# Kernel tuning notes

Hardware: AMD Instinct MI355X
Metric: run time of the kernel (lower is better)

## Reference

```python
import jax, jax.numpy as jnp
import numpy as np

DEPTH = 5  # init kwarg


def setup_inputs() -> dict:
    key = jax.random.key(0)
    ks = jax.random.split(key, 10)
    n_atoms, n_bonds, hidden, n_mols = 80000, 160001, 448, 4000
    ATOM_DIM, BOND_DIM = 38, 11
    inp = {
        "fatoms": jax.random.normal(ks[0], (n_atoms, ATOM_DIM), jnp.float32),
        "fbonds": jax.random.normal(ks[1], (n_bonds, ATOM_DIM + BOND_DIM), jnp.float32),
        "W_i": jax.random.normal(ks[2], (ATOM_DIM + BOND_DIM, hidden), jnp.float32) * 0.1,
        "W_h": jax.random.normal(ks[3], (hidden, hidden), jnp.float32) * 0.05,
        "W_o": jax.random.normal(ks[4], (ATOM_DIM + hidden, hidden), jnp.float32) * 0.05,
        "b_o": jax.random.normal(ks[5], (hidden,), jnp.float32),
        "agraph": jax.random.randint(ks[6], (n_atoms, 6), 0, n_bonds, jnp.int64),
        "bgraph": jax.random.randint(ks[7], (n_bonds, 6), 0, n_bonds, jnp.int64),
        "mol_idx": jnp.sort(jax.random.randint(ks[8], (n_atoms,), 0, n_mols, jnp.int64)),
        "n_mols": n_mols,
    }
    return inp


def reference(fatoms, fbonds, W_i, W_h, W_o, b_o, agraph, bgraph, mol_idx, n_mols):
    # binput: [n_bonds, hidden]
    binput = fbonds @ W_i
    message = jax.nn.relu(binput)
    for _ in range(DEPTH - 1):
        # padded-neighbor gather-sum over MAX_NB=6, then linear + relu
        nei = jnp.take(message, bgraph, axis=0).sum(axis=1)  # [n_bonds, hidden]
        message = jax.nn.relu(binput + nei @ W_h)
    # atom readout
    nei = jnp.take(message, agraph, axis=0).sum(axis=1)  # [n_atoms, hidden]
    ainput = jnp.concatenate([fatoms, nei], axis=1)
    atom_hiddens = jax.nn.relu(ainput @ W_o + b_o)
    # per-molecule mean pooling (scope -> segment ids)
    sums = jax.ops.segment_sum(atom_hiddens, mol_idx, num_segments=n_mols)
    counts = jax.ops.segment_sum(jnp.ones((atom_hiddens.shape[0],), atom_hiddens.dtype), mol_idx, num_segments=n_mols)
    return sums / jnp.maximum(counts, 1.0)[:, None]
```

## Files before the change

kernel.cpp:

```cpp
#include <hip/hip_runtime.h>

#define HIDDEN 448

typedef __attribute__((ext_vector_type(8))) short short8;
typedef __attribute__((ext_vector_type(4))) float f32x4;

__device__ __forceinline__ unsigned short f2bf(float f) {
    unsigned int u = __float_as_uint(f);
    u = (u + 0x7fffu + ((u >> 16) & 1u)) >> 16;
    return (unsigned short)u;
}
__device__ __forceinline__ float bf2f(unsigned short h) {
    return __uint_as_float(((unsigned int)h) << 16);
}
__device__ __forceinline__ unsigned int cvt_pk_bf16(float a, float b) {
    unsigned int r;
    asm("v_cvt_pk_bf16_f32 %0, %1, %2" : "=v"(r) : "v"(a), "v"(b));
    return r;
}
__device__ __forceinline__ void async16(void* lds, const void* g) {
    __builtin_amdgcn_global_load_lds(
        (const __attribute__((address_space(1))) unsigned int*)g,
        (__attribute__((address_space(3))) unsigned int*)lds, 16, 0, 0);
}

__global__ __launch_bounds__(256) void prep_wcat_kernel(
    const float* __restrict__ Wtop, int Ktop, const float* __restrict__ Wbot,
    unsigned short* __restrict__ out)
{
    const int idx = blockIdx.x * 256 + threadIdx.x;
    if (idx >= 448 * 512) return;
    const int n = idx >> 9, k = idx & 511;
    float v = 0.0f;
    if (k < Ktop) v = Wtop[k * HIDDEN + n];
    else if (k >= 64) v = Wbot[(k - 64) * HIDDEN + n];
    out[(size_t)n * 512 + (k ^ (((n >> 1) & 3) << 3))] = f2bf(v);
}

__global__ __launch_bounds__(256) void prep_apad_kernel(
    const float* __restrict__ A, int K, unsigned short* __restrict__ out,
    int Mreal, int total)
{
    const int idx = blockIdx.x * 256 + threadIdx.x;
    if (idx >= total) return;
    const int row = idx >> 6, k = idx & 63;
    const float v = (row < Mreal && k < K) ? A[(size_t)row * K + k] : 0.0f;
    out[(size_t)row * 64 + (k ^ (((row >> 1) & 3) << 3))] = f2bf(v);
}

template<int GRAPH, int OUTQ>
__global__ __launch_bounds__(512, 4) void gemm_mfma_kernel(
    const unsigned short* __restrict__ Apad,
    const unsigned char* __restrict__ Xq,
    const float* __restrict__ Xs,
    const int* __restrict__ graph,
    const unsigned short* __restrict__ BT,
    const float* __restrict__ bias,
    unsigned short* outh,
    unsigned char* __restrict__ outq,
    float* __restrict__ outs,
    int M, int nsteps)
{
    __shared__ __align__(16) unsigned char smem[37888];
    unsigned short* As = (unsigned short*)smem;
    unsigned short* Bs = (unsigned short*)(smem + 8192);
    float* rmaxbuf = (float*)(smem + 36864);

    const int tid = threadIdx.x, lane = tid & 63, wv = tid >> 6;
    const int row0 = blockIdx.x * 64;
    const int wrow = (wv & 1) * 32;
    const int wcol = (wv >> 1) * 112;
    const int rr = lane & 15, ch = lane >> 4;
    const int lrow = lane >> 2, lq = lane & 3;

    const int arow = tid >> 3, asub = tid & 7;
    const int ah = asub >> 2, ac = asub & 3;
    const int awaddr = arow * 64 + ah * 32 + ((ac ^ ((arow >> 1) & 3)) << 3);

    int goff[6]; float gscl[6];
    uint2 pf[6];
    if (GRAPH) {
        const int grow = row0 + arow;
        const bool ok = grow < M;
        #pragma unroll
        for (int j = 0; j < 6; ++j) {
            const int gj = ok ? graph[(size_t)grow * 6 + j] : 0;
            goff[j] = gj * 448;
            gscl[j] = ok ? Xs[gj] : 0.0f;
        }
        #pragma unroll
        for (int j = 0; j < 6; ++j)
            pf[j] = *(const uint2*)(Xq + goff[j] + asub * 8);
    }

    f32x4 acc[2][7] = {};

    for (int s = 0; s < nsteps; ++s) {
        #pragma unroll
        for (int i = 0; i < 4; ++i) {
            const int t = wv + 8 * i;
            if (t < 28)
                async16(Bs + t * 512 + lane * 8,
                        BT + (size_t)(t * 16 + lrow) * 512 + s * 32 + lq * 8);
        }
        if (s == 0) {
            async16(As + wv * 512 + lane * 8,
                    Apad + (size_t)(row0 + wv * 8) * 64 + lane * 8);
        } else if (GRAPH && s >= 2 && !((s - 2) & 1)) {
            const uint2 b0 = pf[0], b1 = pf[1], b2 = pf[2],
                        b3 = pf[3], b4 = pf[4], b5 = pf[5];
            float a0 = 0, a1 = 0, a2 = 0, a3 = 0, a4 = 0, a5 = 0, a6 = 0, a7 = 0;
            #pragma unroll
            for (int j = 0; j < 6; ++j) {
                const uint2 b = (j == 0) ? b0 : (j == 1) ? b1 : (j == 2) ? b2
                              : (j == 3) ? b3 : (j == 4) ? b4 : b5;
                const float sc = gscl[j];
                a0 += (float)(b.x & 255u) * sc;
                a1 += (float)((b.x >> 8) & 255u) * sc;
                a2 += (float)((b.x >> 16) & 255u) * sc;
                a3 += (float)(b.x >> 24) * sc;
                a4 += (float)(b.y & 255u) * sc;
                a5 += (float)((b.y >> 8) & 255u) * sc;
                a6 += (float)((b.y >> 16) & 255u) * sc;
                a7 += (float)(b.y >> 24) * sc;
            }
            uint4 w;
            w.x = cvt_pk_bf16(a0, a1);
            w.y = cvt_pk_bf16(a2, a3);
            w.z = cvt_pk_bf16(a4, a5);
            w.w = cvt_pk_bf16(a6, a7);
            *(uint4*)&As[awaddr] = w;
            const int nxt = ((s - 2) >> 1) + 1;
            if (nxt < 7) {
                #pragma unroll
                for (int j = 0; j < 6; ++j)
                    pf[j] = *(const uint2*)(Xq + goff[j] + nxt * 64 + asub * 8);
            }
        }
        __syncthreads();

        const int hoff = (s & 1) * 32;
        short8 av[2];
        #pragma unroll
        for (int m = 0; m < 2; ++m) {
            const int r = wrow + m * 16 + rr;
            av[m] = *(const short8*)&As[r * 64 + hoff + ((ch ^ ((r >> 1) & 3)) << 3)];
        }
        #pragma unroll
        for (int n = 0; n < 7; ++n) {
            const int cl = wcol + n * 16 + rr;
            const short8 bv = *(const short8*)&Bs[cl * 32 + ((ch ^ ((cl >> 1) & 3)) << 3)];
            #pragma unroll
            for (int m = 0; m < 2; ++m)
                acc[m][n] = __builtin_amdgcn_mfma_f32_16x16x32_bf16(
                    av[m], bv, acc[m][n], 0, 0, 0);
        }
        __syncthreads();
    }

    const int r4 = ch << 2;

    if (OUTQ) {
        float rpm[2][4];
        #pragma unroll
        for (int m = 0; m < 2; ++m)
            #pragma unroll
            for (int j = 0; j < 4; ++j) {
                float mx = 0.0f;
                #pragma unroll
                for (int n = 0; n < 7; ++n) mx = fmaxf(mx, acc[m][n][j]);
                rpm[m][j] = mx;
            }
        #pragma unroll
        for (int off = 1; off < 16; off <<= 1)
            #pragma unroll
            for (int m = 0; m < 2; ++m)
                #pragma unroll
                for (int j = 0; j < 4; ++j)
                    rpm[m][j] = fmaxf(rpm[m][j], __shfl_xor(rpm[m][j], off));
        if (rr == 0)
            #pragma unroll
            for (int m = 0; m < 2; ++m)
                #pragma unroll
                for (int j = 0; j < 4; ++j)
                    rmaxbuf[(wrow + m * 16 + r4 + j) * 4 + (wv >> 1)] = rpm[m][j];
        __syncthreads();
        float inv[2][4];
        #pragma unroll
        for (int m = 0; m < 2; ++m)
            #pragma unroll
            for (int j = 0; j < 4; ++j) {
                const int rl = wrow + m * 16 + r4 + j;
                const float mx = fmaxf(fmaxf(rmaxbuf[rl * 4 + 0], rmaxbuf[rl * 4 + 1]),
                                       fmaxf(rmaxbuf[rl * 4 + 2], rmaxbuf[rl * 4 + 3]));
                inv[m][j] = (mx > 0.0f) ? (255.0f / mx) : 0.0f;
                if (wv < 2 && rr == 0 && row0 + rl < M)
                    outs[row0 + rl] = mx * (1.0f / 255.0f);
            }
        __syncthreads();
        unsigned char* q8 = smem;
        #pragma unroll
        for (int m = 0; m < 2; ++m)
            #pragma unroll
            for (int j = 0; j < 4; ++j) {
                const int rl = wrow + m * 16 + r4 + j;
                #pragma unroll
                for (int n = 0; n < 7; ++n) {
                    const float v = fmaxf(acc[m][n][j], 0.0f);
                    q8[rl * 448 + wcol + n * 16 + rr] =
                        (unsigned char)__float2uint_rn(fminf(v * inv[m][j], 255.0f));
                }
            }
        __syncthreads();
        #pragma unroll
        for (int i = 0; i < 4; ++i) {
            const int u = tid + 512 * i;
            if (u < 1792 && row0 + u / 28 < M)
                ((uint4*)(outq + (size_t)row0 * 448))[u] = ((const uint4*)q8)[u];
        }
    } else {
        #pragma unroll
        for (int n = 0; n < 7; ++n) {
            const int col = wcol + n * 16 + rr;
            const float bsv = bias ? bias[col] : 0.0f;
            #pragma unroll
            for (int m = 0; m < 2; ++m)
                #pragma unroll
                for (int j = 0; j < 4; ++j) {
                    const int row = row0 + wrow + m * 16 + r4 + j;
                    if (row < M)
                        outh[(size_t)row * HIDDEN + col] =
                            f2bf(fmaxf(acc[m][n][j] + bsv, 0.0f));
                }
        }
    }
}

__global__ void segmean_kernel(
    const unsigned short* __restrict__ ah, const int* __restrict__ mol_idx,
    float* __restrict__ out, int n_atoms)
{
    const int m = blockIdx.x;
    const int c = threadIdx.x;
    int l = 0, r = n_atoms;
    while (l < r) { const int mid = (l + r) >> 1; if (mol_idx[mid] < m) l = mid + 1; else r = mid; }
    const int start = l;
    r = n_atoms;
    while (l < r) { const int mid = (l + r) >> 1; if (mol_idx[mid] < m + 1) l = mid + 1; else r = mid; }
    const int end = l;
    float acc = 0.0f;
    for (int a = start; a < end; ++a) acc += bf2f(ah[(size_t)a * HIDDEN + c]);
    out[(size_t)m * HIDDEN + c] = acc / fmaxf((float)(end - start), 1.0f);
}

__global__ __launch_bounds__(256) void fill_kernel(float* __restrict__ out, int n, float val)
{
    const int i = blockIdx.x * 256 + threadIdx.x;
    if (i < n) out[i] = val;
}

extern "C" void kernel_launch(void* const* d_in, const int* in_sizes, int n_in,
                              void* d_out, int out_size, void* d_ws, size_t ws_size,
                              hipStream_t stream)
{
    const float* fatoms = (const float*)d_in[0];
    const float* fbonds = (const float*)d_in[1];
    const float* W_i    = (const float*)d_in[2];
    const float* W_h    = (const float*)d_in[3];
    const float* W_o    = (const float*)d_in[4];
    const float* b_o    = (const float*)d_in[5];
    const int*   agraph = (const int*)d_in[6];
    const int*   bgraph = (const int*)d_in[7];
    const int*   mol_idx= (const int*)d_in[8];

    const int n_atoms = in_sizes[0] / 38;
    const int n_bonds = in_sizes[1] / 49;
    const int n_mols  = out_size / HIDDEN;

    const int Mb_b = (n_bonds + 63) & ~63;
    const int Mb_a = (n_atoms + 63) & ~63;

    const size_t eW  = (size_t)448 * 512;
    const size_t eFb = (size_t)Mb_b * 64;
    const size_t eFa = (size_t)Mb_a * 64;
    const size_t eX  = (size_t)Mb_b * 448;

    const size_t need = 2 * eW * 2 + eFb * 2 + eFa * 2 +
                        2 * eX + 2 * (size_t)Mb_b * 4;

    const dim3 blk(256);

    if (ws_size >= need) {
        unsigned short* WhcatT  = (unsigned short*)d_ws;
        unsigned short* WocatT  = WhcatT + eW;
        unsigned short* fbondsP = WocatT + eW;
        unsigned short* fatomsP = fbondsP + eFb;
        unsigned char*  Xq0     = (unsigned char*)(fatomsP + eFa);
        unsigned char*  Xq1     = Xq0 + eX;
        float*          Xs0     = (float*)(Xq1 + eX);
        float*          Xs1     = Xs0 + Mb_b;

        const int wblocks = (448 * 512 + 255) / 256;
        hipLaunchKernelGGL(prep_wcat_kernel, dim3(wblocks), blk, 0, stream,
                           W_i, 49, W_h, WhcatT);
        hipLaunchKernelGGL(prep_wcat_kernel, dim3(wblocks), blk, 0, stream,
                           W_o, 38, W_o + 38 * HIDDEN, WocatT);
        hipLaunchKernelGGL(prep_apad_kernel, dim3(((int)eFb + 255) / 256), blk, 0, stream,
                           fbonds, 49, fbondsP, n_bonds, (int)eFb);
        hipLaunchKernelGGL(prep_apad_kernel, dim3(((int)eFa + 255) / 256), blk, 0, stream,
                           fatoms, 38, fatomsP, n_atoms, (int)eFa);

        const dim3 gB(Mb_b / 64), gA(Mb_a / 64), tpb(512);

        unsigned char* Xq[2] = {Xq0, Xq1};
        float*         Xs[2] = {Xs0, Xs1};

        hipLaunchKernelGGL((gemm_mfma_kernel<0, 1>), gB, tpb, 0, stream,
                           fbondsP, (const unsigned char*)nullptr, (const float*)nullptr,
                           (const int*)nullptr, WhcatT, (const float*)nullptr,
                           (unsigned short*)nullptr, Xq[0], Xs[0], n_bonds, 2);
        int p = 0;
        for (int it = 0; it < 4; ++it) {
            hipLaunchKernelGGL((gemm_mfma_kernel<1, 1>), gB, tpb, 0, stream,
                               fbondsP, Xq[p], Xs[p], bgraph, WhcatT,
                               (const float*)nullptr, (unsigned short*)nullptr,
                               Xq[p ^ 1], Xs[p ^ 1], n_bonds, 16);
            p ^= 1;
        }
        unsigned short* ah = (unsigned short*)Xq[p ^ 1];
        hipLaunchKernelGGL((gemm_mfma_kernel<1, 0>), gA, tpb, 0, stream,
                           fatomsP, Xq[p], Xs[p], agraph, WocatT, b_o,
                           ah, (unsigned char*)nullptr, (float*)nullptr, n_atoms, 16);
        hipLaunchKernelGGL(segmean_kernel, dim3(n_mols), dim3(HIDDEN), 0, stream,
                           ah, mol_idx, (float*)d_out, n_atoms);
    } else {
        const float val = -(float)((double)ws_size / (1024.0 * 1024.0));
        hipLaunchKernelGGL(fill_kernel, dim3((out_size + 255) / 256), blk, 0, stream,
                           (float*)d_out, out_size, val);
    }
}
```

Before: 928.3 us.

## Double-buffer A and B LDS tiles in GEMM to overlap loads with MFMA

Splits LDS into two B buffers and two A buffers so the next K-step's weight tile and gathered activations are staged while the current step's MFMAs run. This removes one of the two barriers per step. The step count becomes a compile-time constant so the loop can be fully specialized. LDS per block roughly doubles, which can lower the number of resident blocks per CU and reduce latency hiding for the gather loads.

```diff
diff --git a/kernel.cpp b/kernel.cpp
--- a/kernel.cpp
+++ b/kernel.cpp
@@ -59,12 +59,11 @@
     unsigned short* outh,
     unsigned char* __restrict__ outq,
     float* __restrict__ outs,
-    int M, int nsteps)
-{
-    __shared__ __align__(16) unsigned char smem[37888];
-    unsigned short* As = (unsigned short*)smem;
-    unsigned short* Bs = (unsigned short*)(smem + 8192);
-    float* rmaxbuf = (float*)(smem + 36864);
+    int M)
+{
+    constexpr int NSTEPS = GRAPH ? 16 : 2;
+    __shared__ __align__(16) unsigned char smem[74752];
+    float* rmaxbuf = (float*)(smem + 73728);
 
     const int tid = threadIdx.x, lane = tid & 63, wv = tid >> 6;
     const int row0 = blockIdx.x * 64;
@@ -74,11 +73,10 @@
     const int lrow = lane >> 2, lq = lane & 3;
 
     const int arow = tid >> 3, asub = tid & 7;
-    const int ah = asub >> 2, ac = asub & 3;
-    const int awaddr = arow * 64 + ah * 32 + ((ac ^ ((arow >> 1) & 3)) << 3);
-
-    int goff[6]; float gscl[6];
-    uint2 pf[6];
+    const int ahh = asub >> 2, ac = asub & 3;
+    const int awoff = arow * 64 + ahh * 32 + ((ac ^ ((arow >> 1) & 3)) << 3);
+
+    int goff[6]; float gscl[6]; uint2 pf[6];
     if (GRAPH) {
         const int grow = row0 + arow;
         const bool ok = grow < M;
@@ -93,27 +91,58 @@
             pf[j] = *(const uint2*)(Xq + goff[j] + asub * 8);
     }
 
-    f32x4 acc[2][7] = {};
-
-    for (int s = 0; s < nsteps; ++s) {
+    {
+        unsigned short* Bs0 = (unsigned short*)(smem + 16384);
         #pragma unroll
         for (int i = 0; i < 4; ++i) {
             const int t = wv + 8 * i;
             if (t < 28)
-                async16(Bs + t * 512 + lane * 8,
-                        BT + (size_t)(t * 16 + lrow) * 512 + s * 32 + lq * 8);
-        }
-        if (s == 0) {
-            async16(As + wv * 512 + lane * 8,
-                    Apad + (size_t)(row0 + wv * 8) * 64 + lane * 8);
-        } else if (GRAPH && s >= 2 && !((s - 2) & 1)) {
-            const uint2 b0 = pf[0], b1 = pf[1], b2 = pf[2],
-                        b3 = pf[3], b4 = pf[4], b5 = pf[5];
+                async16(Bs0 + t * 512 + lane * 8,
+                        BT + (size_t)(t * 16 + lrow) * 512 + lq * 8);
+        }
+        unsigned short* As0 = (unsigned short*)smem;
+        async16(As0 + wv * 512 + lane * 8,
+                Apad + (size_t)(row0 + wv * 8) * 64 + lane * 8);
+    }
+    __syncthreads();
+
+    f32x4 acc[2][7] = {};
+
+    for (int s = 0; s < NSTEPS; ++s) {
+        unsigned short* BsCur = (unsigned short*)(smem + 16384 + (size_t)(s & 1) * 28672);
+        unsigned short* AsCur = (unsigned short*)(smem + (size_t)((s >> 1) & 1) * 8192);
+
+        if (s + 1 < NSTEPS) {
+            unsigned short* BsNxt =
+                (unsigned short*)(smem + 16384 + (size_t)((s + 1) & 1) * 28672);
+            #pragma unroll
+            for (int i = 0; i < 4; ++i) {
+                const int t = wv + 8 * i;
+                if (t < 28)
+                    async16(BsNxt + t * 512 + lane * 8,
+                            BT + (size_t)(t * 16 + lrow) * 512 + (s + 1) * 32 + lq * 8);
+            }
+        }
+
+        const int hoff = (s & 1) * 32;
+        short8 av[2], bv[7];
+        #pragma unroll
+        for (int m = 0; m < 2; ++m) {
+            const int r = wrow + m * 16 + rr;
+            av[m] = *(const short8*)&AsCur[r * 64 + hoff + ((ch ^ ((r >> 1) & 3)) << 3)];
+        }
+        #pragma unroll
+        for (int n = 0; n < 7; ++n) {
+            const int cl = wcol + n * 16 + rr;
+            bv[n] = *(const short8*)&BsCur[cl * 32 + ((ch ^ ((cl >> 1) & 3)) << 3)];
+        }
+
+        if (GRAPH && !(s & 1) && s <= 12) {
+            const int p = s >> 1;
             float a0 = 0, a1 = 0, a2 = 0, a3 = 0, a4 = 0, a5 = 0, a6 = 0, a7 = 0;
             #pragma unroll
             for (int j = 0; j < 6; ++j) {
-                const uint2 b = (j == 0) ? b0 : (j == 1) ? b1 : (j == 2) ? b2
-                              : (j == 3) ? b3 : (j == 4) ? b4 : b5;
+                const uint2 b = pf[j];
                 const float sc = gscl[j];
                 a0 += (float)(b.x & 255u) * sc;
                 a1 += (float)((b.x >> 8) & 255u) * sc;
@@ -129,32 +158,23 @@
             w.y = cvt_pk_bf16(a2, a3);
             w.z = cvt_pk_bf16(a4, a5);
             w.w = cvt_pk_bf16(a6, a7);
-            *(uint4*)&As[awaddr] = w;
-            const int nxt = ((s - 2) >> 1) + 1;
-            if (nxt < 7) {
+            unsigned short* AsNxt =
+                (unsigned short*)(smem + (size_t)((p + 1) & 1) * 8192);
+            *(uint4*)&AsNxt[awoff] = w;
+            if (s <= 10) {
                 #pragma unroll
                 for (int j = 0; j < 6; ++j)
-                    pf[j] = *(const uint2*)(Xq + goff[j] + nxt * 64 + asub * 8);
-            }
-        }
-        __syncthreads();
-
-        const int hoff = (s & 1) * 32;
-        short8 av[2];
-        #pragma unroll
-        for (int m = 0; m < 2; ++m) {
-            const int r = wrow + m * 16 + rr;
-            av[m] = *(const short8*)&As[r * 64 + hoff + ((ch ^ ((r >> 1) & 3)) << 3)];
-        }
-        #pragma unroll
-        for (int n = 0; n < 7; ++n) {
-            const int cl = wcol + n * 16 + rr;
-            const short8 bv = *(const short8*)&Bs[cl * 32 + ((ch ^ ((cl >> 1) & 3)) << 3)];
+                    pf[j] = *(const uint2*)(Xq + goff[j] + (p + 1) * 64 + asub * 8);
+            }
+        }
+
+        #pragma unroll
+        for (int n = 0; n < 7; ++n)
             #pragma unroll
             for (int m = 0; m < 2; ++m)
                 acc[m][n] = __builtin_amdgcn_mfma_f32_16x16x32_bf16(
-                    av[m], bv, acc[m][n], 0, 0, 0);
-        }
+                    av[m], bv[n], acc[m][n], 0, 0, 0);
+
         __syncthreads();
     }
 
@@ -318,19 +338,19 @@
         hipLaunchKernelGGL((gemm_mfma_kernel<0, 1>), gB, tpb, 0, stream,
                            fbondsP, (const unsigned char*)nullptr, (const float*)nullptr,
                            (const int*)nullptr, WhcatT, (const float*)nullptr,
-                           (unsigned short*)nullptr, Xq[0], Xs[0], n_bonds, 2);
+                           (unsigned short*)nullptr, Xq[0], Xs[0], n_bonds);
         int p = 0;
         for (int it = 0; it < 4; ++it) {
             hipLaunchKernelGGL((gemm_mfma_kernel<1, 1>), gB, tpb, 0, stream,
                                fbondsP, Xq[p], Xs[p], bgraph, WhcatT,
                                (const float*)nullptr, (unsigned short*)nullptr,
-                               Xq[p ^ 1], Xs[p ^ 1], n_bonds, 16);
+                               Xq[p ^ 1], Xs[p ^ 1], n_bonds);
             p ^= 1;
         }
         unsigned short* ah = (unsigned short*)Xq[p ^ 1];
         hipLaunchKernelGGL((gemm_mfma_kernel<1, 0>), gA, tpb, 0, stream,
                            fatomsP, Xq[p], Xs[p], agraph, WocatT, b_o,
-                           ah, (unsigned char*)nullptr, (float*)nullptr, n_atoms, 16);
+                           ah, (unsigned char*)nullptr, (float*)nullptr, n_atoms);
         hipLaunchKernelGGL(segmean_kernel, dim3(n_mols), dim3(HIDDEN), 0, stream,
                            ah, mol_idx, (float*)d_out, n_atoms);
     } else {
```

Result: slower. 1.664 ms (+79.2%).

## Overlap neighbor-gather loads and dequant-sum with MFMA in the fused gather GEMM

Applied to the files above, without the earlier changes.

Restructures the K-loop schedule so the gathered int8 neighbor rows are loaded after the barrier on even steps. The dequantize-and-sum runs on odd steps after the MFMAs have been issued, and the packed bf16 result is held in a register and written to LDS at the start of the next even step. All B fragments are now loaded from LDS before the MFMA sequence begins. The goal is to hide global gather latency and the scalar accumulation behind matrix work rather than stalling before the barrier. In exchange it holds more live registers (bv[7], wreg), which could lower occupancy.

```diff
diff --git a/kernel.cpp b/kernel.cpp
--- a/kernel.cpp
+++ b/kernel.cpp
@@ -74,11 +74,10 @@
     const int lrow = lane >> 2, lq = lane & 3;
 
     const int arow = tid >> 3, asub = tid & 7;
-    const int ah = asub >> 2, ac = asub & 3;
-    const int awaddr = arow * 64 + ah * 32 + ((ac ^ ((arow >> 1) & 3)) << 3);
-
-    int goff[6]; float gscl[6];
-    uint2 pf[6];
+    const int ahh = asub >> 2, ac = asub & 3;
+    const int awoff = arow * 64 + ahh * 32 + ((ac ^ ((arow >> 1) & 3)) << 3);
+
+    int goff[6]; float gscl[6]; uint2 pf[6]; uint4 wreg;
     if (GRAPH) {
         const int grow = row0 + arow;
         const bool ok = grow < M;
@@ -88,14 +87,13 @@
             goff[j] = gj * 448;
             gscl[j] = ok ? Xs[gj] : 0.0f;
         }
-        #pragma unroll
-        for (int j = 0; j < 6; ++j)
-            pf[j] = *(const uint2*)(Xq + goff[j] + asub * 8);
     }
 
     f32x4 acc[2][7] = {};
 
     for (int s = 0; s < nsteps; ++s) {
+        if (GRAPH && s >= 2 && !(s & 1))
+            *(uint4*)&As[awoff] = wreg;
         #pragma unroll
         for (int i = 0; i < 4; ++i) {
             const int t = wv + 8 * i;
@@ -103,17 +101,42 @@
                 async16(Bs + t * 512 + lane * 8,
                         BT + (size_t)(t * 16 + lrow) * 512 + s * 32 + lq * 8);
         }
-        if (s == 0) {
+        if (s == 0)
             async16(As + wv * 512 + lane * 8,
                     Apad + (size_t)(row0 + wv * 8) * 64 + lane * 8);
-        } else if (GRAPH && s >= 2 && !((s - 2) & 1)) {
-            const uint2 b0 = pf[0], b1 = pf[1], b2 = pf[2],
-                        b3 = pf[3], b4 = pf[4], b5 = pf[5];
+        __syncthreads();
+
+        if (GRAPH && !(s & 1) && s <= 12) {
+            const int pb = (s >> 1) * 64;
+            #pragma unroll
+            for (int j = 0; j < 6; ++j)
+                pf[j] = *(const uint2*)(Xq + goff[j] + pb + asub * 8);
+        }
+
+        const int hoff = (s & 1) * 32;
+        short8 av[2], bv[7];
+        #pragma unroll
+        for (int m = 0; m < 2; ++m) {
+            const int r = wrow + m * 16 + rr;
+            av[m] = *(const short8*)&As[r * 64 + hoff + ((ch ^ ((r >> 1) & 3)) << 3)];
+        }
+        #pragma unroll
+        for (int n = 0; n < 7; ++n) {
+            const int cl = wcol + n * 16 + rr;
+            bv[n] = *(const short8*)&Bs[cl * 32 + ((ch ^ ((cl >> 1) & 3)) << 3)];
+        }
+        #pragma unroll
+        for (int n = 0; n < 7; ++n)
+            #pragma unroll
+            for (int m = 0; m < 2; ++m)
+                acc[m][n] = __builtin_amdgcn_mfma_f32_16x16x32_bf16(
+                    av[m], bv[n], acc[m][n], 0, 0, 0);
+
+        if (GRAPH && (s & 1) && s <= 13) {
             float a0 = 0, a1 = 0, a2 = 0, a3 = 0, a4 = 0, a5 = 0, a6 = 0, a7 = 0;
             #pragma unroll
             for (int j = 0; j < 6; ++j) {
-                const uint2 b = (j == 0) ? b0 : (j == 1) ? b1 : (j == 2) ? b2
-                              : (j == 3) ? b3 : (j == 4) ? b4 : b5;
+                const uint2 b = pf[j];
                 const float sc = gscl[j];
                 a0 += (float)(b.x & 255u) * sc;
                 a1 += (float)((b.x >> 8) & 255u) * sc;
@@ -124,36 +147,10 @@
                 a6 += (float)((b.y >> 16) & 255u) * sc;
                 a7 += (float)(b.y >> 24) * sc;
             }
-            uint4 w;
-            w.x = cvt_pk_bf16(a0, a1);
-            w.y = cvt_pk_bf16(a2, a3);
-            w.z = cvt_pk_bf16(a4, a5);
-            w.w = cvt_pk_bf16(a6, a7);
-            *(uint4*)&As[awaddr] = w;
-            const int nxt = ((s - 2) >> 1) + 1;
-            if (nxt < 7) {
-                #pragma unroll
-                for (int j = 0; j < 6; ++j)
-                    pf[j] = *(const uint2*)(Xq + goff[j] + nxt * 64 + asub * 8);
-            }
-        }
-        __syncthreads();
-
-        const int hoff = (s & 1) * 32;
-        short8 av[2];
-        #pragma unroll
-        for (int m = 0; m < 2; ++m) {
-            const int r = wrow + m * 16 + rr;
-            av[m] = *(const short8*)&As[r * 64 + hoff + ((ch ^ ((r >> 1) & 3)) << 3)];
-        }
-        #pragma unroll
-        for (int n = 0; n < 7; ++n) {
-            const int cl = wcol + n * 16 + rr;
-            const short8 bv = *(const short8*)&Bs[cl * 32 + ((ch ^ ((cl >> 1) & 3)) << 3)];
-            #pragma unroll
-            for (int m = 0; m < 2; ++m)
-                acc[m][n] = __builtin_amdgcn_mfma_f32_16x16x32_bf16(
-                    av[m], bv, acc[m][n], 0, 0, 0);
+            wreg.x = cvt_pk_bf16(a0, a1);
+            wreg.y = cvt_pk_bf16(a2, a3);
+            wreg.z = cvt_pk_bf16(a4, a5);
+            wreg.w = cvt_pk_bf16(a6, a7);
         }
         __syncthreads();
     }
```

New measurement: 1.014 ms. 1.09x slower.
